# Optimization experiments

Hardware: AMD Instinct MI355X
Metric: run time of the kernel (lower is better)

The kernel has to match this reference:

```python
import jax, jax.numpy as jnp
import numpy as np

B, S, E = 2, 2048, 1024
H = 32
DK = E // H  # 32, must equal H for the bilinear einsum to type-check
FFN = 4096
EPS = 1e-5


def layer_norm(x, g, b):
    m = jnp.mean(x, axis=-1, keepdims=True)
    v = jnp.mean((x - m) ** 2, axis=-1, keepdims=True)
    return (x - m) * jax.lax.rsqrt(v + EPS) * g + b


def setup_inputs() -> dict:
    key = jax.random.key(0)
    ks = jax.random.split(key, 16)
    sc = lambda fan_in: 1.0 / np.sqrt(fan_in)
    return {
        "x": jax.random.normal(ks[0], (B, S, E), jnp.float32),
        "Wq": jax.random.normal(ks[1], (E, E), jnp.float32) * sc(E),
        "bq": jax.random.normal(ks[2], (E,), jnp.float32) * 0.02,
        "Wk": jax.random.normal(ks[3], (E, E), jnp.float32) * sc(E),
        "bk": jax.random.normal(ks[4], (E,), jnp.float32) * 0.02,
        "Wv": jax.random.normal(ks[5], (E, E), jnp.float32) * sc(E),
        "bv": jax.random.normal(ks[6], (E,), jnp.float32) * 0.02,
        "kernelW": jax.random.normal(ks[7], (DK, H), jnp.float32),
        "Wo": jax.random.normal(ks[8], (E, E), jnp.float32) * sc(E),
        "bo": jax.random.normal(ks[9], (E,), jnp.float32) * 0.02,
        "W1": jax.random.normal(ks[10], (E, FFN), jnp.float32) * sc(E),
        "b1": jax.random.normal(ks[11], (FFN,), jnp.float32) * 0.02,
        "W2": jax.random.normal(ks[12], (FFN, E), jnp.float32) * sc(FFN),
        "b2": jax.random.normal(ks[13], (E,), jnp.float32) * 0.02,
        "g1": jnp.ones((E,), jnp.float32),
        "beta1": jnp.zeros((E,), jnp.float32),
        "g2": jnp.ones((E,), jnp.float32),
        "beta2": jnp.zeros((E,), jnp.float32),
    }


def reference(x, Wq, bq, Wk, bk, Wv, bv, kernelW, Wo, bo, W1, b1, W2, b2, g1, beta1, g2, beta2):
    # projections -> [B, H, S, DK]
    split = lambda t: t.reshape(B, S, H, DK).transpose(0, 2, 1, 3)
    q = split(x @ Wq + bq)
    k = split(x @ Wk + bk)
    v = split(x @ Wv + bv)
    # bilinear quantum-kernel score: sim[b,h,i,j] = sum_d q[b,h,i,d]*W[d,h]*k[b,h,j,d]
    sim = jnp.einsum('bhqd,dh,bhkd->bhqk', q, kernelW, k)
    attn = jax.nn.softmax(sim, axis=-1)  # dropout is identity at eval
    out = jnp.matmul(attn, v)  # [B, H, S, DK]
    out = out.transpose(0, 2, 1, 3).reshape(B, S, E) @ Wo + bo
    x = layer_norm(x + out, g1, beta1)
    ffn = jax.nn.relu(x @ W1 + b1) @ W2 + b2
    return layer_norm(x + ffn, g2, beta2)
```

## Files before the change

kernel.cpp:

```cpp
#include <hip/hip_runtime.h>


typedef unsigned short u16;
typedef unsigned int u32;
typedef __bf16 bf16x8 __attribute__((ext_vector_type(8)));
typedef float f32x4 __attribute__((ext_vector_type(4)));
typedef float f32x16 __attribute__((ext_vector_type(16)));

__device__ __forceinline__ u16 f2b(float f) {
  union { float f; unsigned u; } x; x.f = f;
  unsigned r = x.u + 0x7FFFu + ((x.u >> 16) & 1u);
  return (u16)(r >> 16);
}

__device__ __forceinline__ float b2f(u16 u) {
  union { u32 u; float f; } x; x.u = (u32)u << 16; return x.f;
}

__device__ __forceinline__ unsigned pkbf(float lo, float hi) {
  unsigned r;
  asm("v_cvt_pk_bf16_f32 %0, %1, %2" : "=v"(r) : "v"(lo), "v"(hi));
  return r;
}

__device__ __forceinline__ float expo2(float x) {
#if __has_builtin(__builtin_amdgcn_exp2f)
  return __builtin_amdgcn_exp2f(x);
#else
  return exp2f(x);
#endif
}

#define GLDS16(gp, lp)                                                         \
  __builtin_amdgcn_global_load_lds(                                            \
      (const __attribute__((address_space(1))) void*)(gp),                     \
      (__attribute__((address_space(3))) void*)(lp), 16, 0, 0)

__global__ __launch_bounds__(256) void prep_kernel(
    const float* __restrict__ Wq, const float* __restrict__ Wk,
    const float* __restrict__ Wv, const float* __restrict__ Wo,
    const float* __restrict__ W1, const float* __restrict__ W2,
    const float* __restrict__ x, u16* __restrict__ WqT, u16* __restrict__ WoT,
    u16* __restrict__ W1T, u16* __restrict__ W2T, u16* __restrict__ xb) {
  __shared__ float tile[32][33];
  const int id = blockIdx.x;
  if (id < 12288) {
    const float* W; u16* WT; int K, N, bx, by;
    if (id < 4096) {
      const int w = id >> 10, local = id & 1023;
      bx = local & 31; by = local >> 5; K = 1024; N = 1024;
      W = (w == 0) ? Wq : (w == 1) ? Wk : (w == 2) ? Wv : Wo;
      WT = (w == 0) ? WqT : (w == 1) ? WqT + 1048576
           : (w == 2) ? WqT + 2097152 : WoT;
    } else if (id < 8192) {
      const int local = id - 4096;
      bx = local & 127; by = local >> 7; K = 1024; N = 4096;
      W = W1; WT = W1T;
    } else {
      const int local = id - 8192;
      bx = local & 31; by = local >> 5; K = 4096; N = 1024;
      W = W2; WT = W2T;
    }
    const int tx = threadIdx.x & 31, ty = threadIdx.x >> 5;
    const int n0 = bx * 32, k0 = by * 32;
#pragma unroll
    for (int i = 0; i < 4; ++i)
      tile[ty + 8 * i][tx] = W[(size_t)(k0 + ty + 8 * i) * N + n0 + tx];
    __syncthreads();
#pragma unroll
    for (int i = 0; i < 4; ++i)
      WT[(size_t)(n0 + ty + 8 * i) * K + k0 + tx] = f2b(tile[tx][ty + 8 * i]);
  } else {
    const int i = (id - 12288) * 256 + threadIdx.x;
    float4 v = ((const float4*)x)[i];
    ushort4 o;
    o.x = f2b(v.x); o.y = f2b(v.y); o.z = f2b(v.z); o.w = f2b(v.w);
    ((ushort4*)xb)[i] = o;
  }
}

template <int MODE, int BN>
__global__ __launch_bounds__(256) void gemmT(
    const u16* __restrict__ A, const u16* __restrict__ BT,
    const float* __restrict__ bias, const float* __restrict__ bias2,
    const float* __restrict__ bias3, const float* __restrict__ res,
    void* __restrict__ outp, const float* __restrict__ kW, int N_, int K_) {
  constexpr int ABYT = 128 * 32 * 2;
  constexpr int BBYT = BN * 32 * 2;
  constexpr int STRIDE = ABYT + BBYT;
  constexpr int MI = (BN == 128) ? 4 : 2;
  __shared__ __align__(16) char SH[2 * STRIDE];
  const int t = threadIdx.x, lane = t & 63, wid = t >> 6;
  const int gx = gridDim.x;
  const int id = blockIdx.y * gx + blockIdx.x;
  const int nb = gx * gridDim.y;
  const int sid = (id & 7) * (nb >> 3) + (id >> 3);
  const int bx = sid % gx;
  int by = sid / gx;
  int kh6 = 0;
  if constexpr (MODE == 6) { kh6 = by >> 5; by &= 31; }
  const int m0 = by * 128, n0 = bx * BN;
  const int wr = (BN == 128) ? (wid >> 1) * 64 : wid * 32;
  const int wc = (BN == 128) ? (wid & 1) * 64 : 0;
  const int lr = lane & 15, lg = lane >> 4;
  const int K = K_;
  const int koff = (MODE == 6) ? kh6 * 1024 : 0;

  f32x4 acc[MI][4] = {};

  const u16* ga0 = A + (size_t)(m0 + (t >> 2)) * K + koff + (t & 3) * 8;
  const u16* ga1 = ga0 + (size_t)64 * K;
  const u16* gb0 = BT + (size_t)(n0 + (t >> 2)) * K + koff + (t & 3) * 8;
  const u16* gb1 = gb0 + (size_t)64 * K;
  const int stA = wid * 1024;

#define STAGE(CUR, KT)                                                         \
  {                                                                            \
    char* l_ = (char*)SH + (CUR) * STRIDE + stA;                               \
    const size_t o_ = (size_t)(KT) * 32;                                       \
    GLDS16(ga0 + o_, l_);                                                      \
    GLDS16(ga1 + o_, l_ + 4096);                                               \
    GLDS16(gb0 + o_, l_ + ABYT);                                               \
    if constexpr (BN == 128) GLDS16(gb1 + o_, l_ + ABYT + 4096);               \
  }

  const int nk = (MODE == 6) ? 32 : (K >> 5);
  STAGE(0, 0);
  __syncthreads();
  int cur = 0;
  for (int kt = 0; kt < nk; ++kt) {
    if (kt + 1 < nk) STAGE(cur ^ 1, kt + 1);
    const char* l = (const char*)SH + cur * STRIDE;
    bf16x8 af[MI], bf[4];
#pragma unroll
    for (int i = 0; i < MI; ++i)
      af[i] = *(const bf16x8*)(l + (wr + i * 16 + lr) * 64 + lg * 16);
#pragma unroll
    for (int i = 0; i < 4; ++i)
      bf[i] = *(const bf16x8*)(l + ABYT + (wc + i * 16 + lr) * 64 + lg * 16);
#pragma unroll
    for (int mi = 0; mi < MI; ++mi)
#pragma unroll
      for (int ni = 0; ni < 4; ++ni)
        acc[mi][ni] = __builtin_amdgcn_mfma_f32_16x16x32_bf16(
            af[mi], bf[ni], acc[mi][ni], 0, 0, 0);
    __syncthreads();
    cur ^= 1;
  }
#undef STAGE

#pragma unroll
  for (int mi = 0; mi < MI; ++mi) {
#pragma unroll
    for (int ni = 0; ni < 4; ++ni) {
      const int row = m0 + wr + mi * 16 + lg * 4;
      const int col = n0 + wc + ni * 16 + lr;
      f32x4 v = acc[mi][ni];
      if constexpr (MODE == 2) {
        const float bv = bias[col];
        u16* o = (u16*)outp;
        const u16* rb = (const u16*)res;
#pragma unroll
        for (int r = 0; r < 4; ++r) {
          const int rr = row + r;
          o[(size_t)rr * N_ + col] =
              f2b(v[r] + bv + b2f(rb[(size_t)rr * N_ + col]));
        }
      } else if constexpr (MODE == 3) {
        const float bv = bias[col];
        u16* o = (u16*)outp;
#pragma unroll
        for (int r = 0; r < 4; ++r) {
          const int rr = row + r;
          float y = v[r] + bv;
          o[(size_t)rr * N_ + col] = f2b(y > 0.f ? y : 0.f);
        }
      } else if constexpr (MODE == 6) {
        u16* o = (kh6 < 2) ? ((u16*)outp + (size_t)kh6 * 4194304)
                           : ((u16*)res + (size_t)(kh6 - 2) * 4194304);
#pragma unroll
        for (int r = 0; r < 4; ++r) {
          const int rr = row + r;
          o[(size_t)rr * N_ + col] = f2b(v[r]);
        }
      } else {
        const int proj = col >> 10, c = col & 1023;
        const int h = c >> 5, d = c & 31;
        u16* qout = (u16*)outp;
        if (proj == 0) {
          const float bv = bias[c];
          const float sc = kW[d * 32 + h] * 1.44269504089f;
#pragma unroll
          for (int r = 0; r < 4; ++r) {
            const int rr = row + r;
            const int bb = rr >> 11, s = rr & 2047;
            qout[(size_t)(((bb * 32 + h) * 2048) + s) * 32 + d] =
                f2b((v[r] + bv) * sc);
          }
        } else if (proj == 1) {
          const float bv = bias2[c];
          u16* kout = qout + 4194304;
          const int c2 = d >> 3;
#pragma unroll
          for (int r = 0; r < 4; ++r) {
            const int rr = row + r;
            const int bb = rr >> 11, s = rr & 2047;
            const int k = s & 63;
            const int g = ((k >> 5) << 1) | (c2 >> 1);
            kout[(size_t)(bb * 32 + h) * 65536 + (s >> 6) * 2048 + g * 512 +
                 (c2 & 1) * 256 + (k & 31) * 8 + (d & 7)] = f2b(v[r] + bv);
          }
        } else {
          const float bv = bias3[c];
          u16* vout = qout + 8388608;
          const int bb = row >> 11, s0 = row & 2047;
          const int k = s0 & 63;
          const int cc = k >> 3, rb = cc >> 1, hb = cc & 1, e = k & 7;
          ushort4 st;
          st.x = f2b(v[0] + bv); st.y = f2b(v[1] + bv);
          st.z = f2b(v[2] + bv); st.w = f2b(v[3] + bv);
          *(ushort4*)(vout + (size_t)(bb * 32 + h) * 65536 +
                      (s0 >> 6) * 2048 + rb * 512 + hb * 256 + d * 8 + e) = st;
        }
      }
    }
  }
}

__device__ __forceinline__ void attn_tile(
    const bf16x8& k0, const bf16x8& k1, const bf16x8& k2, const bf16x8& k3,
    const bf16x8& v0, const bf16x8& v1, const bf16x8& v2, const bf16x8& v3,
    const bf16x8& qb0, const bf16x8& qb1,
    f32x16& acc, float& la, float& lb, float& lc, float& ld) {
  const f32x16 z16 = {};
  f32x16 s0 = __builtin_amdgcn_mfma_f32_32x32x16_bf16(k0, qb0, z16, 0, 0, 0);
  s0 = __builtin_amdgcn_mfma_f32_32x32x16_bf16(k1, qb1, s0, 0, 0, 0);
  f32x16 s1 = __builtin_amdgcn_mfma_f32_32x32x16_bf16(k2, qb0, z16, 0, 0, 0);
  s1 = __builtin_amdgcn_mfma_f32_32x32x16_bf16(k3, qb1, s1, 0, 0, 0);
  float p0[16], p1[16];
#pragma unroll
  for (int r = 0; r < 16; ++r) p0[r] = expo2(s0[r]);
#pragma unroll
  for (int r = 0; r < 16; ++r) p1[r] = expo2(s1[r]);
#pragma unroll
  for (int r = 0; r < 4; ++r) {
    la += p0[r] + p1[r];
    lb += p0[4 + r] + p1[4 + r];
    lc += p0[8 + r] + p1[8 + r];
    ld += p0[12 + r] + p1[12 + r];
  }
  {
    u32 x0 = pkbf(p0[0], p0[1]), x1 = pkbf(p0[2], p0[3]);
    u32 y0 = pkbf(p0[4], p0[5]), y1 = pkbf(p0[6], p0[7]);
    asm("v_permlane32_swap_b32 %0, %1" : "+v"(x0), "+v"(y0));
    asm("v_permlane32_swap_b32 %0, %1" : "+v"(x1), "+v"(y1));
    union { u32 d[4]; bf16x8 v; } u;
    u.d[0] = x0; u.d[1] = x1; u.d[2] = y0; u.d[3] = y1;
    acc = __builtin_amdgcn_mfma_f32_32x32x16_bf16(v0, u.v, acc, 0, 0, 0);
  }
  {
    u32 x0 = pkbf(p0[8], p0[9]), x1 = pkbf(p0[10], p0[11]);
    u32 y0 = pkbf(p0[12], p0[13]), y1 = pkbf(p0[14], p0[15]);
    asm("v_permlane32_swap_b32 %0, %1" : "+v"(x0), "+v"(y0));
    asm("v_permlane32_swap_b32 %0, %1" : "+v"(x1), "+v"(y1));
    union { u32 d[4]; bf16x8 v; } u;
    u.d[0] = x0; u.d[1] = x1; u.d[2] = y0; u.d[3] = y1;
    acc = __builtin_amdgcn_mfma_f32_32x32x16_bf16(v1, u.v, acc, 0, 0, 0);
  }
  {
    u32 x0 = pkbf(p1[0], p1[1]), x1 = pkbf(p1[2], p1[3]);
    u32 y0 = pkbf(p1[4], p1[5]), y1 = pkbf(p1[6], p1[7]);
    asm("v_permlane32_swap_b32 %0, %1" : "+v"(x0), "+v"(y0));
    asm("v_permlane32_swap_b32 %0, %1" : "+v"(x1), "+v"(y1));
    union { u32 d[4]; bf16x8 v; } u;
    u.d[0] = x0; u.d[1] = x1; u.d[2] = y0; u.d[3] = y1;
    acc = __builtin_amdgcn_mfma_f32_32x32x16_bf16(v2, u.v, acc, 0, 0, 0);
  }
  {
    u32 x0 = pkbf(p1[8], p1[9]), x1 = pkbf(p1[10], p1[11]);
    u32 y0 = pkbf(p1[12], p1[13]), y1 = pkbf(p1[14], p1[15]);
    asm("v_permlane32_swap_b32 %0, %1" : "+v"(x0), "+v"(y0));
    asm("v_permlane32_swap_b32 %0, %1" : "+v"(x1), "+v"(y1));
    union { u32 d[4]; bf16x8 v; } u;
    u.d[0] = x0; u.d[1] = x1; u.d[2] = y0; u.d[3] = y1;
    acc = __builtin_amdgcn_mfma_f32_32x32x16_bf16(v3, u.v, acc, 0, 0, 0);
  }
}

__global__ __launch_bounds__(512) void attn_kernel(
    const u16* __restrict__ Q, const u16* __restrict__ K,
    const u16* __restrict__ VT, u16* __restrict__ O) {
  __shared__ __align__(16) char LDSB[32768];
  const int t = threadIdx.x, wid = t >> 6, lane = t & 63;
  const int qg = wid & 3, kh = wid >> 2;
  const int bid = blockIdx.x;
  const int swz = (bid & 7) * 128 + (bid >> 3);
  const int bh = swz >> 4;
  const int qt = swz & 15;
  const int q0 = qt * 128 + qg * 32;
  const int lq = lane & 31, hi = lane >> 5;
  const u16* Qh = Q + (size_t)bh * 65536;
  const u16* Kh = K + (size_t)bh * 65536;
  const u16* Vh = VT + (size_t)bh * 65536;

  const bf16x8 qb0 = *(const bf16x8*)(Qh + (size_t)(q0 + lq) * 32 + hi * 8);
  const bf16x8 qb1 = *(const bf16x8*)(Qh + (size_t)(q0 + lq) * 32 + 16 + hi * 8);

  const u16* kg = Kh + wid * 512 + lane * 8;
  const u16* vg = Vh + wid * 512 + lane * 8;
  const int lds_w = wid * 1024;

#define STAGEA(CUR, I)                                                         \
  if (wid < 4) {                                                               \
    char* b_ = LDSB + (CUR) * 16384 + lds_w;                                   \
    GLDS16(kg + (size_t)(I) * 2048, b_);                                       \
    GLDS16(vg + (size_t)(I) * 2048, b_ + 4096);                                \
    GLDS16(kg + (size_t)(16 + (I)) * 2048, b_ + 8192);                         \
    GLDS16(vg + (size_t)(16 + (I)) * 2048, b_ + 12288);                        \
  }

  f32x16 acc = {};
  float la = 0.f, lb = 0.f, lc = 0.f, ld = 0.f;

  STAGEA(0, 0);
  __syncthreads();
  int cur = 0;
#pragma unroll 1
  for (int i = 0; i < 16; ++i) {
    if (i < 15) STAGEA(cur ^ 1, i + 1);
    const char* kb = LDSB + cur * 16384 + kh * 8192 + lane * 16;
    const bf16x8 ka0 = *(const bf16x8*)(kb);
    const bf16x8 ka1 = *(const bf16x8*)(kb + 1024);
    const bf16x8 ka2 = *(const bf16x8*)(kb + 2048);
    const bf16x8 ka3 = *(const bf16x8*)(kb + 3072);
    const bf16x8 va0 = *(const bf16x8*)(kb + 4096);
    const bf16x8 va1 = *(const bf16x8*)(kb + 5120);
    const bf16x8 va2 = *(const bf16x8*)(kb + 6144);
    const bf16x8 va3 = *(const bf16x8*)(kb + 7168);
    attn_tile(ka0, ka1, ka2, ka3, va0, va1, va2, va3, qb0, qb1,
              acc, la, lb, lc, ld);
    __syncthreads();
    cur ^= 1;
  }
#undef STAGEA

  float lrun = (la + lb) + (lc + ld);
  lrun += __shfl_xor(lrun, 32);

  float* sm_acc = (float*)LDSB;
  float* sm_l = (float*)(LDSB + 16384);
  if (kh == 1) {
    sm_l[qg * 32 + lq] = lrun;
#pragma unroll
    for (int r = 0; r < 16; ++r) sm_acc[(qg * 64 + lane) * 16 + r] = acc[r];
  }
  __syncthreads();
  if (kh == 0) {
    const float inv = 1.f / (lrun + sm_l[qg * 32 + lq]);
    const int bb = bh >> 5, h = bh & 31;
    u16* o = O + (size_t)(bb * 2048 + q0 + lq) * 1024 + h * 32;
#pragma unroll
    for (int g = 0; g < 4; ++g) {
      ushort4 st;
      st.x = f2b((acc[g * 4 + 0] + sm_acc[(qg * 64 + lane) * 16 + g * 4 + 0]) * inv);
      st.y = f2b((acc[g * 4 + 1] + sm_acc[(qg * 64 + lane) * 16 + g * 4 + 1]) * inv);
      st.z = f2b((acc[g * 4 + 2] + sm_acc[(qg * 64 + lane) * 16 + g * 4 + 2]) * inv);
      st.w = f2b((acc[g * 4 + 3] + sm_acc[(qg * 64 + lane) * 16 + g * 4 + 3]) * inv);
      *(ushort4*)(o + g * 8 + hi * 4) = st;
    }
  }
}

__global__ __launch_bounds__(256) void ln1b_kernel(
    u16* __restrict__ X, const float* __restrict__ g,
    const float* __restrict__ b) {
  const int wid = threadIdx.x >> 6, lane = threadIdx.x & 63;
  const int row = blockIdx.x * 4 + wid;
  ushort4* X4 = (ushort4*)(X + (size_t)row * 1024);
  float4 xs[4];
  float s = 0.f, sq = 0.f;
#pragma unroll
  for (int i = 0; i < 4; ++i) {
    const ushort4 u = X4[lane + i * 64];
    float4 v;
    v.x = b2f(u.x); v.y = b2f(u.y); v.z = b2f(u.z); v.w = b2f(u.w);
    xs[i] = v;
    s += v.x + v.y + v.z + v.w;
    sq += v.x * v.x + v.y * v.y + v.z * v.z + v.w * v.w;
  }
#pragma unroll
  for (int m = 1; m < 64; m <<= 1) { s += __shfl_xor(s, m); sq += __shfl_xor(sq, m); }
  const float mean = s * (1.f / 1024.f);
  float var = sq * (1.f / 1024.f) - mean * mean;
  var = var > 0.f ? var : 0.f;
  const float rstd = rsqrtf(var + 1e-5f);
  const float4* g4 = (const float4*)g;
  const float4* b4 = (const float4*)b;
#pragma unroll
  for (int i = 0; i < 4; ++i) {
    const int c = lane + i * 64;
    const float4 gv = g4[c], bv = b4[c], x = xs[i];
    ushort4 yb;
    yb.x = f2b((x.x - mean) * rstd * gv.x + bv.x);
    yb.y = f2b((x.y - mean) * rstd * gv.y + bv.y);
    yb.z = f2b((x.z - mean) * rstd * gv.z + bv.z);
    yb.w = f2b((x.w - mean) * rstd * gv.w + bv.w);
    X4[c] = yb;
  }
}

__global__ __launch_bounds__(256) void ln2sum_kernel(
    const u16* __restrict__ P0, const u16* __restrict__ P1,
    const u16* __restrict__ P2, const u16* __restrict__ P3,
    const u16* __restrict__ R, const float* __restrict__ bias,
    const float* __restrict__ g, const float* __restrict__ b,
    float* __restrict__ out) {
  const int wid = threadIdx.x >> 6, lane = threadIdx.x & 63;
  const int row = blockIdx.x * 4 + wid;
  const ushort4* A4 = (const ushort4*)(P0 + (size_t)row * 1024);
  const ushort4* B4 = (const ushort4*)(P1 + (size_t)row * 1024);
  const ushort4* C4 = (const ushort4*)(P2 + (size_t)row * 1024);
  const ushort4* D4 = (const ushort4*)(P3 + (size_t)row * 1024);
  const ushort4* R4 = (const ushort4*)(R + (size_t)row * 1024);
  const float4* Bi4 = (const float4*)bias;
  float4 xs[4];
  float s = 0.f, sq = 0.f;
#pragma unroll
  for (int i = 0; i < 4; ++i) {
    const int c = lane + i * 64;
    const ushort4 a = A4[c], pb = B4[c], pc = C4[c], pd = D4[c], rr = R4[c];
    const float4 bi = Bi4[c];
    float4 x;
    x.x = (b2f(a.x) + b2f(pb.x)) + (b2f(pc.x) + b2f(pd.x)) + b2f(rr.x) + bi.x;
    x.y = (b2f(a.y) + b2f(pb.y)) + (b2f(pc.y) + b2f(pd.y)) + b2f(rr.y) + bi.y;
    x.z = (b2f(a.z) + b2f(pb.z)) + (b2f(pc.z) + b2f(pd.z)) + b2f(rr.z) + bi.z;
    x.w = (b2f(a.w) + b2f(pb.w)) + (b2f(pc.w) + b2f(pd.w)) + b2f(rr.w) + bi.w;
    xs[i] = x;
    s += x.x + x.y + x.z + x.w;
    sq += x.x * x.x + x.y * x.y + x.z * x.z + x.w * x.w;
  }
#pragma unroll
  for (int m = 1; m < 64; m <<= 1) { s += __shfl_xor(s, m); sq += __shfl_xor(sq, m); }
  const float mean = s * (1.f / 1024.f);
  float var = sq * (1.f / 1024.f) - mean * mean;
  var = var > 0.f ? var : 0.f;
  const float rstd = rsqrtf(var + 1e-5f);
  const float4* g4 = (const float4*)g;
  const float4* b4 = (const float4*)b;
  float4* of = (float4*)(out + (size_t)row * 1024);
#pragma unroll
  for (int i = 0; i < 4; ++i) {
    const int c = lane + i * 64;
    const float4 gv = g4[c], bv = b4[c], x = xs[i];
    float4 y;
    y.x = (x.x - mean) * rstd * gv.x + bv.x;
    y.y = (x.y - mean) * rstd * gv.y + bv.y;
    y.z = (x.z - mean) * rstd * gv.z + bv.z;
    y.w = (x.w - mean) * rstd * gv.w + bv.w;
    of[c] = y;
  }
}

extern "C" void kernel_launch(void* const* d_in, const int* in_sizes, int n_in,
                              void* d_out, int out_size, void* d_ws,
                              size_t ws_size, hipStream_t stream) {
  const float* x   = (const float*)d_in[0];
  const float* Wq  = (const float*)d_in[1];
  const float* bq  = (const float*)d_in[2];
  const float* Wk  = (const float*)d_in[3];
  const float* bk  = (const float*)d_in[4];
  const float* Wv  = (const float*)d_in[5];
  const float* bv  = (const float*)d_in[6];
  const float* kW  = (const float*)d_in[7];
  const float* Wo  = (const float*)d_in[8];
  const float* bo  = (const float*)d_in[9];
  const float* W1  = (const float*)d_in[10];
  const float* b1  = (const float*)d_in[11];
  const float* W2  = (const float*)d_in[12];
  const float* b2  = (const float*)d_in[13];
  const float* g1  = (const float*)d_in[14];
  const float* be1 = (const float*)d_in[15];
  const float* g2  = (const float*)d_in[16];
  const float* be2 = (const float*)d_in[17];

  char* ws = (char*)d_ws;
  const size_t MB = 1024 * 1024;
  u16*   WqT = (u16*)(ws + 0 * MB);
  u16*   WoT = (u16*)(ws + 6 * MB);
  u16*   W1T = (u16*)(ws + 8 * MB);
  u16*   W2T = (u16*)(ws + 16 * MB);
  u16*   r1b = (u16*)(ws + 24 * MB);
  u16*   xb  = (u16*)(ws + 40 * MB);
  u16*   qhB = (u16*)(ws + 48 * MB);
  u16*   khB = (u16*)(ws + 56 * MB);
  u16*   vTB = (u16*)(ws + 64 * MB);
  u16*   hf  = (u16*)(ws + 40 * MB);
  u16*   ao  = (u16*)(ws + 72 * MB);
  u16*   p0  = (u16*)(ws + 0 * MB);
  u16*   p2  = (u16*)(ws + 72 * MB);

  const dim3 blk(256);

  prep_kernel<<<16384, blk, 0, stream>>>(Wq, Wk, Wv, Wo, W1, W2, x,
                                         WqT, WoT, W1T, W2T, xb);

  gemmT<5, 128><<<dim3(24, 32), blk, 0, stream>>>(
      xb, WqT, bq, bk, bv, nullptr, qhB, kW, 3072, 1024);

  attn_kernel<<<1024, dim3(512), 0, stream>>>(qhB, khB, vTB, ao);

  gemmT<2, 64><<<dim3(16, 32), blk, 0, stream>>>(
      ao, WoT, bo, nullptr, nullptr, (const float*)xb, r1b, nullptr,
      1024, 1024);
  ln1b_kernel<<<1024, blk, 0, stream>>>(r1b, g1, be1);
  gemmT<3, 128><<<dim3(32, 32), blk, 0, stream>>>(
      r1b, W1T, b1, nullptr, nullptr, nullptr, hf, nullptr, 4096, 1024);
  gemmT<6, 128><<<dim3(8, 128), blk, 0, stream>>>(
      hf, W2T, nullptr, nullptr, nullptr, (const float*)p2, p0, nullptr,
      1024, 4096);
  ln2sum_kernel<<<1024, blk, 0, stream>>>(p0, p0 + 4194304, p2, p2 + 4194304,
                                          r1b, b2, g2, be2, (float*)d_out);

  (void)in_sizes; (void)n_in; (void)out_size; (void)ws_size;
}
```

Measured before the change: 235.9 us.

## Triple-buffer K/V LDS staging in attention with explicit vmcnt waits

Changes the attention kernel's K/V staging from a double buffer to a three-slot ring buffer in LDS, prefetching two tiles ahead. The full __syncthreads is replaced by raw s_barrier pairs around a partial s_waitcnt vmcnt, so global-to-LDS loads stay in flight across iterations. This is meant to hide global load latency better. In exchange LDS use grows from 32KB to 48KB per block, which can lower occupancy, and correctness depends on the vmcnt counts matching the number of outstanding loads.

```diff
diff --git a/kernel.cpp b/kernel.cpp
--- a/kernel.cpp
+++ b/kernel.cpp
@@ -290,7 +290,7 @@
 __global__ __launch_bounds__(512) void attn_kernel(
     const u16* __restrict__ Q, const u16* __restrict__ K,
     const u16* __restrict__ VT, u16* __restrict__ O) {
-  __shared__ __align__(16) char LDSB[32768];
+  __shared__ __align__(16) char LDSB[49152];
   const int t = threadIdx.x, wid = t >> 6, lane = t & 63;
   const int qg = wid & 3, kh = wid >> 2;
   const int bid = blockIdx.x;
@@ -310,45 +310,60 @@
   const u16* vg = Vh + wid * 512 + lane * 8;
   const int lds_w = wid * 1024;
 
-#define STAGEA(CUR, I)                                                         \
+#define STAGEA(SLOT, I)                                                        \
   if (wid < 4) {                                                               \
-    char* b_ = LDSB + (CUR) * 16384 + lds_w;                                   \
+    char* b_ = LDSB + (SLOT) * 16384 + lds_w;                                  \
     GLDS16(kg + (size_t)(I) * 2048, b_);                                       \
     GLDS16(vg + (size_t)(I) * 2048, b_ + 4096);                                \
     GLDS16(kg + (size_t)(16 + (I)) * 2048, b_ + 8192);                         \
     GLDS16(vg + (size_t)(16 + (I)) * 2048, b_ + 12288);                        \
   }
 
+#define COMPUTE(SLOT)                                                          \
+  {                                                                            \
+    const char* kb = LDSB + (SLOT) * 16384 + kh * 8192 + lane * 16;            \
+    const bf16x8 ka0 = *(const bf16x8*)(kb);                                   \
+    const bf16x8 ka1 = *(const bf16x8*)(kb + 1024);                            \
+    const bf16x8 ka2 = *(const bf16x8*)(kb + 2048);                            \
+    const bf16x8 ka3 = *(const bf16x8*)(kb + 3072);                            \
+    const bf16x8 va0 = *(const bf16x8*)(kb + 4096);                            \
+    const bf16x8 va1 = *(const bf16x8*)(kb + 5120);                            \
+    const bf16x8 va2 = *(const bf16x8*)(kb + 6144);                            \
+    const bf16x8 va3 = *(const bf16x8*)(kb + 7168);                            \
+    attn_tile(ka0, ka1, ka2, ka3, va0, va1, va2, va3, qb0, qb1,                \
+              acc, la, lb, lc, ld);                                            \
+  }
+
   f32x16 acc = {};
   float la = 0.f, lb = 0.f, lc = 0.f, ld = 0.f;
 
   STAGEA(0, 0);
-  __syncthreads();
-  int cur = 0;
+  STAGEA(1, 1);
 #pragma unroll 1
-  for (int i = 0; i < 16; ++i) {
-    if (i < 15) STAGEA(cur ^ 1, i + 1);
-    const char* kb = LDSB + cur * 16384 + kh * 8192 + lane * 16;
-    const bf16x8 ka0 = *(const bf16x8*)(kb);
-    const bf16x8 ka1 = *(const bf16x8*)(kb + 1024);
-    const bf16x8 ka2 = *(const bf16x8*)(kb + 2048);
-    const bf16x8 ka3 = *(const bf16x8*)(kb + 3072);
-    const bf16x8 va0 = *(const bf16x8*)(kb + 4096);
-    const bf16x8 va1 = *(const bf16x8*)(kb + 5120);
-    const bf16x8 va2 = *(const bf16x8*)(kb + 6144);
-    const bf16x8 va3 = *(const bf16x8*)(kb + 7168);
-    attn_tile(ka0, ka1, ka2, ka3, va0, va1, va2, va3, qb0, qb1,
-              acc, la, lb, lc, ld);
-    __syncthreads();
-    cur ^= 1;
-  }
+  for (int i = 0; i < 14; ++i) {
+    __builtin_amdgcn_s_barrier();
+    STAGEA((i + 2) % 3, i + 2);
+    asm volatile("s_waitcnt vmcnt(8)" ::: "memory");
+    __builtin_amdgcn_s_barrier();
+    COMPUTE(i % 3);
+  }
+  __builtin_amdgcn_s_barrier();
+  asm volatile("s_waitcnt vmcnt(4)" ::: "memory");
+  __builtin_amdgcn_s_barrier();
+  COMPUTE(2);
+  __builtin_amdgcn_s_barrier();
+  asm volatile("s_waitcnt vmcnt(0)" ::: "memory");
+  __builtin_amdgcn_s_barrier();
+  COMPUTE(0);
 #undef STAGEA
+#undef COMPUTE
 
   float lrun = (la + lb) + (lc + ld);
   lrun += __shfl_xor(lrun, 32);
 
-  float* sm_acc = (float*)LDSB;
-  float* sm_l = (float*)(LDSB + 16384);
+  __syncthreads();
+  float* sm_acc = (float*)(LDSB + 16384);
+  float* sm_l = (float*)(LDSB + 32768);
   if (kh == 1) {
     sm_l[qg * 32 + lq] = lrun;
 #pragma unroll
```

Result: no change. 237.1 us (+0.5%).
